# Kernel optimization log

Hardware: AMD Instinct MI355X
Metric: run time of the kernel (lower is better)

## Reference

```python
import jax, jax.numpy as jnp
import numpy as np

N_NODES = 100000
N_EDGES = 800000
IN_FEATS = 128
OUT_FEATS = 128
RANK_DIM = 128
NUM_BOND_TYPES = 32


def setup_inputs() -> dict:
    key = jax.random.key(0)
    ks = jax.random.split(key, 8)
    feat = jax.random.normal(ks[0], (N_NODES, IN_FEATS), dtype=jnp.float32)
    src = jax.random.randint(ks[1], (N_EDGES,), 0, N_NODES)
    dst = jax.random.randint(ks[2], (N_EDGES,), 0, N_NODES)
    # guarantee every node has in-degree >= 1 (module forbids 0-in-degree nodes)
    dst = dst.at[:N_NODES].set(jnp.arange(N_NODES))
    edge_attr = jax.random.randint(ks[3], (N_EDGES,), 0, NUM_BOND_TYPES)
    # xavier-uniform-like params
    def xavier(k, shape):
        lim = float(np.sqrt(6.0 / (shape[0] + shape[1])))
        return jax.random.uniform(k, shape, jnp.float32, -lim, lim)
    w1 = xavier(ks[4], (IN_FEATS, OUT_FEATS))
    w2 = xavier(ks[5], (IN_FEATS + 1, RANK_DIM))
    v = xavier(ks[6], (RANK_DIM, OUT_FEATS))
    bond_emb = jax.random.normal(ks[7], (NUM_BOND_TYPES, OUT_FEATS), dtype=jnp.float32)
    return {"feat": feat, "src": src, "dst": dst, "edge_attr": edge_attr,
            "w1": w1, "w2": w2, "v": v, "bond_emb": bond_emb}


def reference(feat, src, dst, edge_attr, w1, w2, v, bond_emb):
    N = feat.shape[0]
    E = src.shape[0]
    ones_e = jnp.ones((E,), dtype=feat.dtype)
    # norm == 'both': scale source features by out_degree^{-1/2}
    out_deg = jnp.clip(jax.ops.segment_sum(ones_e, src, num_segments=N), 1.0)
    feat_src = feat * (out_deg ** -0.5)[:, None]
    # two small GEMMs on node features
    h_sum = feat_src @ w1  # [N, out]
    feat_aug = jnp.concatenate([feat_src, jnp.ones((N, 1), dtype=feat.dtype)], axis=1)
    h_prod = jnp.tanh(feat_aug @ w2)  # [N, rank]
    # edge embedding (BondEncoder)
    ew = bond_emb[edge_attr]  # [E, out]
    # u_mul_e then neighbor-wise product / sum reductions onto dst
    m_prod = h_prod[src] * ew
    m_sum = h_sum[src] * ew
    hp = jax.ops.segment_prod(m_prod, dst, num_segments=N)
    hs = jax.ops.segment_sum(m_sum, dst, num_segments=N)
    rst = hs + hp @ v
    # norm == 'both': scale result by in_degree^{-1/2}
    in_deg = jnp.clip(jax.ops.segment_sum(ones_e, dst, num_segments=N), 1.0)
    rst = rst * (in_deg ** -0.5)[:, None]
    return rst
```

## Files before the change

kernel.cpp:

```cpp
#include <hip/hip_runtime.h>

#define N_NODES 100000
#define N_EDGES 800000

typedef unsigned short u16;
typedef unsigned int u32;
typedef __attribute__((ext_vector_type(8))) short short8;
typedef __attribute__((ext_vector_type(4))) float floatx4;

#define NBUK 196
#define BSH 9
#define NBLK 782
#define NB_PREPW 192

__device__ __forceinline__ float bflo(u32 u) {
    union { u32 i; float f; } v; v.i = u << 16; return v.f;
}
__device__ __forceinline__ float bfhi(u32 u) {
    union { u32 i; float f; } v; v.i = u & 0xFFFF0000u; return v.f;
}
__device__ __forceinline__ u16 f2bf(float f) {
    union { float f; u32 i; } v; v.f = f;
    u32 r = (v.i + 0x7FFFu + ((v.i >> 16) & 1u)) >> 16;
    return (u16)r;
}
__device__ __forceinline__ float fast_tanh(float x) {
    float e = __expf(2.0f * x);
    return 1.0f - 2.0f * __builtin_amdgcn_rcpf(e + 1.0f);
}


__global__ __launch_bounds__(256) void kA_count(const int* __restrict__ src, const int* __restrict__ dst,
                                                int* __restrict__ countsD, int* __restrict__ countsS,
                                                const float* __restrict__ w1, const float* __restrict__ w2,
                                                const float* __restrict__ v, u16* __restrict__ wvfrag) {
    __shared__ int cd[NBUK], cs[NBUK];
    if (blockIdx.x >= NBLK) {
        int idx = (blockIdx.x - NBLK) * 256 + threadIdx.x;
        if (idx < 3 * 16384) {
            int m = idx >> 14, r = idx & 16383;
            int k = r >> 7, o = r & 127;
            float val = (m == 0) ? w1[k * 128 + o] : (m == 1) ? w2[k * 128 + o] : v[k * 128 + o];
            int ot = o >> 4, ks = k >> 5, quad = (k >> 3) & 3, j = k & 7;
            int lane = (quad << 4) | (o & 15);
            wvfrag[(((m * 8 + ot) * 4 + ks) * 64 + lane) * 8 + j] = f2bf(val);
        }
        return;
    }
    for (int i = threadIdx.x; i < NBUK; i += 256) { cd[i] = 0; cs[i] = 0; }
    __syncthreads();
    int e4 = (blockIdx.x * 256 + threadIdx.x) * 4;
    if (e4 < N_EDGES) {
        int4 d4 = *(const int4*)(dst + e4);
        int4 s4 = *(const int4*)(src + e4);
        atomicAdd(&cd[d4.x >> BSH], 1); atomicAdd(&cd[d4.y >> BSH], 1);
        atomicAdd(&cd[d4.z >> BSH], 1); atomicAdd(&cd[d4.w >> BSH], 1);
        atomicAdd(&cs[s4.x >> BSH], 1); atomicAdd(&cs[s4.y >> BSH], 1);
        atomicAdd(&cs[s4.z >> BSH], 1); atomicAdd(&cs[s4.w >> BSH], 1);
    }
    __syncthreads();
    for (int i = threadIdx.x; i < NBUK; i += 256) {
        countsD[i * NBLK + blockIdx.x] = cd[i];
        countsS[i * NBLK + blockIdx.x] = cs[i];
    }
}


__global__ __launch_bounds__(256) void kA_scan(int* __restrict__ countsD, int* __restrict__ countsS,
                                               int* __restrict__ totD, int* __restrict__ totS) {
    __shared__ int sc[256];
    int b = blockIdx.x;
    int* cnt = (b < NBUK) ? (countsD + b * NBLK) : (countsS + (b - NBUK) * NBLK);
    int t = threadIdx.x;
    int v[4]; int s = 0;
#pragma unroll
    for (int j = 0; j < 4; j++) { int idx = t * 4 + j; v[j] = (idx < NBLK) ? cnt[idx] : 0; s += v[j]; }
    sc[t] = s; __syncthreads();
    for (int off = 1; off < 256; off <<= 1) {
        int x = (t >= off) ? sc[t - off] : 0;
        __syncthreads();
        sc[t] += x;
        __syncthreads();
    }
    int run = sc[t] - s;
#pragma unroll
    for (int j = 0; j < 4; j++) { int idx = t * 4 + j; if (idx < NBLK) { cnt[idx] = run; run += v[j]; } }
    if (t == 255) { if (b < NBUK) totD[b] = sc[255]; else totS[b - NBUK] = sc[255]; }
}


__global__ __launch_bounds__(256) void kA_scanT(const int* __restrict__ totD, const int* __restrict__ totS,
                                                int* __restrict__ baseD, int* __restrict__ baseS) {
    __shared__ int sd[256], ss[256];
    int t = threadIdx.x;
    int vd = (t < NBUK) ? totD[t] : 0;
    int vs = (t < NBUK) ? totS[t] : 0;
    sd[t] = vd; ss[t] = vs; __syncthreads();
    for (int off = 1; off < 256; off <<= 1) {
        int xd = (t >= off) ? sd[t - off] : 0;
        int xs = (t >= off) ? ss[t - off] : 0;
        __syncthreads();
        sd[t] += xd; ss[t] += xs;
        __syncthreads();
    }
    if (t < NBUK) { baseD[t] = sd[t] - vd; baseS[t] = ss[t] - vs; }
}


__global__ __launch_bounds__(256) void kA_scatter(const int* __restrict__ src, const int* __restrict__ dst,
                                                  const int* __restrict__ attr,
                                                  const int* __restrict__ countsD, const int* __restrict__ countsS,
                                                  const int* __restrict__ baseD, const int* __restrict__ baseS,
                                                  uint2* __restrict__ dbuf, int* __restrict__ sbuf) {
    __shared__ int curD[NBUK], curS[NBUK];
    for (int i = threadIdx.x; i < NBUK; i += 256) {
        curD[i] = baseD[i] + countsD[i * NBLK + blockIdx.x];
        curS[i] = baseS[i] + countsS[i * NBLK + blockIdx.x];
    }
    __syncthreads();
    int e4 = (blockIdx.x * 256 + threadIdx.x) * 4;
    if (e4 < N_EDGES) {
        int4 s4 = *(const int4*)(src + e4);
        int4 d4 = *(const int4*)(dst + e4);
        int4 a4 = *(const int4*)(attr + e4);
        int p, d, s, a;
        d = d4.x; s = s4.x; a = a4.x;
        p = atomicAdd(&curD[d >> BSH], 1); dbuf[p] = make_uint2((u32)d, (u32)((s << 5) | a));
        p = atomicAdd(&curS[s >> BSH], 1); sbuf[p] = s;
        d = d4.y; s = s4.y; a = a4.y;
        p = atomicAdd(&curD[d >> BSH], 1); dbuf[p] = make_uint2((u32)d, (u32)((s << 5) | a));
        p = atomicAdd(&curS[s >> BSH], 1); sbuf[p] = s;
        d = d4.z; s = s4.z; a = a4.z;
        p = atomicAdd(&curD[d >> BSH], 1); dbuf[p] = make_uint2((u32)d, (u32)((s << 5) | a));
        p = atomicAdd(&curS[s >> BSH], 1); sbuf[p] = s;
        d = d4.w; s = s4.w; a = a4.w;
        p = atomicAdd(&curD[d >> BSH], 1); dbuf[p] = make_uint2((u32)d, (u32)((s << 5) | a));
        p = atomicAdd(&curS[s >> BSH], 1); sbuf[p] = s;
    }
}


__global__ __launch_bounds__(256) void k_build(const uint2* __restrict__ dbuf, const int* __restrict__ sbuf,
                                               const int* __restrict__ baseD, const int* __restrict__ totD,
                                               const int* __restrict__ baseS, const int* __restrict__ totS,
                                               int* __restrict__ csr_start, int* __restrict__ in_deg,
                                               float* __restrict__ in_scale, float* __restrict__ out_scale,
                                               int* __restrict__ csr_edge) {
    __shared__ int cnt[512];
    __shared__ int aux[512];
    __shared__ int sc[256];
    int t = threadIdx.x;
    if (blockIdx.x >= NBUK) {
        int b = blockIdx.x - NBUK; int nb0 = b << BSH;
        for (int i = t; i < 512; i += 256) cnt[i] = 0;
        __syncthreads();
        int st = baseS[b], n = totS[b];
        for (int i = st + t; i < st + n; i += 256) atomicAdd(&cnt[sbuf[i] - nb0], 1);
        __syncthreads();
        for (int s = t; s < 512; s += 256) {
            int node = nb0 + s;
            if (node < N_NODES) { int c = cnt[s]; if (c < 1) c = 1; out_scale[node] = rsqrtf((float)c); }
        }
        return;
    }
    int b = blockIdx.x; int nb0 = b << BSH;
    for (int i = t; i < 512; i += 256) cnt[i] = 0;
    __syncthreads();
    int st = baseD[b], n = totD[b];
    for (int i = st + t; i < st + n; i += 256) { uint2 r = dbuf[i]; atomicAdd(&cnt[(int)r.x - nb0], 1); }
    __syncthreads();
    int c0 = cnt[2 * t], c1 = cnt[2 * t + 1];
    int s = c0 + c1; sc[t] = s; __syncthreads();
    for (int off = 1; off < 256; off <<= 1) {
        int x = (t >= off) ? sc[t - off] : 0;
        __syncthreads();
        sc[t] += x;
        __syncthreads();
    }
    int excl = sc[t] - s;
    aux[2 * t] = excl; aux[2 * t + 1] = excl + c0;
    int na = nb0 + 2 * t, nbv = nb0 + 2 * t + 1;
    if (na < N_NODES) {
        in_deg[na] = c0; int cc = c0 < 1 ? 1 : c0;
        in_scale[na] = rsqrtf((float)cc); csr_start[na] = st + excl;
    }
    if (nbv < N_NODES) {
        in_deg[nbv] = c1; int cc = c1 < 1 ? 1 : c1;
        in_scale[nbv] = rsqrtf((float)cc); csr_start[nbv] = st + excl + c0;
    }
    __syncthreads();
    for (int i = st + t; i < st + n; i += 256) {
        uint2 r = dbuf[i];
        int pos = atomicAdd(&aux[(int)r.x - nb0], 1);
        csr_edge[st + pos] = (int)r.y;
    }
}


__global__ __launch_bounds__(256) void k_gemm(const float* __restrict__ feat,
                                              const float* __restrict__ out_scale,
                                              const u16* __restrict__ wvfrag,
                                              const float* __restrict__ w2,
                                              u16* __restrict__ hrow) {
    __shared__ u16 ldsw[32768];
    for (int i = threadIdx.x; i < 4096; i += 256)
        ((ulonglong2*)ldsw)[i] = ((const ulonglong2*)wvfrag)[i];
    __syncthreads();
    int wave = threadIdx.x >> 6, lane = threadIdx.x & 63;
    int quad = lane >> 4, l15 = lane & 15;
    const float* bias = w2 + 128 * 128;
    float bias_v[8];
#pragma unroll
    for (int ot = 0; ot < 8; ot++) bias_v[ot] = bias[ot * 16 + l15];
    const int NT = (N_NODES + 63) / 64;
    for (int tile = blockIdx.x; tile < NT; tile += gridDim.x) {
        int nb = tile * 64 + wave * 16;
        int anode = nb + l15; if (anode >= N_NODES) anode = N_NODES - 1;
        float s = out_scale[anode];
        short8 a[4];
#pragma unroll
        for (int ks = 0; ks < 4; ks++) {
            float4 f0 = *(const float4*)(feat + anode * 128 + ks * 32 + quad * 8);
            float4 f1 = *(const float4*)(feat + anode * 128 + ks * 32 + quad * 8 + 4);
            short8 av;
            av[0] = (short)f2bf(f0.x * s); av[1] = (short)f2bf(f0.y * s);
            av[2] = (short)f2bf(f0.z * s); av[3] = (short)f2bf(f0.w * s);
            av[4] = (short)f2bf(f1.x * s); av[5] = (short)f2bf(f1.y * s);
            av[6] = (short)f2bf(f1.z * s); av[7] = (short)f2bf(f1.w * s);
            a[ks] = av;
        }
#pragma unroll
        for (int ot = 0; ot < 8; ot++) {
            floatx4 accS = (floatx4){0.f, 0.f, 0.f, 0.f};
            floatx4 accP = (floatx4){0.f, 0.f, 0.f, 0.f};
#pragma unroll
            for (int ks = 0; ks < 4; ks++) {
                short8 b0 = *(const short8*)&ldsw[((ot * 4 + ks) * 64 + lane) * 8];
                short8 b1 = *(const short8*)&ldsw[16384 + ((ot * 4 + ks) * 64 + lane) * 8];
                accS = __builtin_amdgcn_mfma_f32_16x16x32_bf16(a[ks], b0, accS, 0, 0, 0);
                accP = __builtin_amdgcn_mfma_f32_16x16x32_bf16(a[ks], b1, accP, 0, 0, 0);
            }
            int o = ot * 16 + l15;
#pragma unroll
            for (int r = 0; r < 4; r++) {
                int node = nb + quad * 4 + r;
                if (node < N_NODES) {
                    u32 pv = (u32)f2bf(accS[r]) | ((u32)f2bf(fast_tanh(accP[r] + bias_v[ot])) << 16);
                    *(u32*)(hrow + node * 256 + o * 2) = pv;
                }
            }
        }
    }
}


__global__ __launch_bounds__(256, 8) void k_edge(const int* __restrict__ csr_start, const int* __restrict__ in_deg,
                                                 const int* __restrict__ csr_edge,
                                                 const u16* __restrict__ hrow,
                                                 const float* __restrict__ bond_emb,
                                                 float* __restrict__ out_hs, u16* __restrict__ hp) {
    int wid = (blockIdx.x * 256 + threadIdx.x) >> 6;
    int lane = threadIdx.x & 63;
    int nwaves = (gridDim.x * 256) >> 6;
    const int NPAIR = N_NODES / 2;
    uint2 hC0 = {0, 0}, hC1 = {0, 0};
    float2 eC0 = {0.f, 0.f}, eC1 = {0.f, 0.f};
    for (int pr = wid; pr < NPAIR; pr += nwaves) {
        int n0 = pr * 2, n1 = n0 + 1;
        int st0 = csr_start[n0];
        int2 dd = *(const int2*)(in_deg + n0);
        int d0 = dd.x, d1 = dd.y;
        int st1 = st0 + d0;
        float as0 = 0.f, as1 = 0.f, ap0 = 1.f, ap1 = 1.f;
        float bs0 = 0.f, bs1 = 0.f, bp0 = 1.f, bp1 = 1.f;
        int b0 = 0, b1 = 0;
        while (b0 < d0 || b1 < d1) {
            int c0 = d0 - b0; c0 = c0 < 0 ? 0 : (c0 > 64 ? 64 : c0);
            int c1 = d1 - b1; c1 = c1 < 0 ? 0 : (c1 > 64 ? 64 : c1);
            int pkv0 = 0, pkv1 = 0;
            if (c0 > 0) { int li = lane < c0 ? lane : c0 - 1; pkv0 = csr_edge[st0 + b0 + li]; }
            if (c1 > 0) { int li = lane < c1 ? lane : c1 - 1; pkv1 = csr_edge[st1 + b1 + li]; }
            uint2 hA0 = hC0, hB0 = hC0, hA1 = hC1, hB1 = hC1;
            float2 eA0 = eC0, eB0 = eC0, eA1 = eC1, eB1 = eC1;
            if (c0 > 0) {
                int pk = __builtin_amdgcn_readlane(pkv0, 0);
                hA0 = *(const uint2*)(hrow + (pk >> 5) * 256 + 4 * lane);
                eA0 = *(const float2*)(bond_emb + (pk & 31) * 128 + 2 * lane);
                if (c0 > 1) {
                    pk = __builtin_amdgcn_readlane(pkv0, 1);
                    hB0 = *(const uint2*)(hrow + (pk >> 5) * 256 + 4 * lane);
                    eB0 = *(const float2*)(bond_emb + (pk & 31) * 128 + 2 * lane);
                }
            }
            if (c1 > 0) {
                int pk = __builtin_amdgcn_readlane(pkv1, 0);
                hA1 = *(const uint2*)(hrow + (pk >> 5) * 256 + 4 * lane);
                eA1 = *(const float2*)(bond_emb + (pk & 31) * 128 + 2 * lane);
                if (c1 > 1) {
                    pk = __builtin_amdgcn_readlane(pkv1, 1);
                    hB1 = *(const uint2*)(hrow + (pk >> 5) * 256 + 4 * lane);
                    eB1 = *(const float2*)(bond_emb + (pk & 31) * 128 + 2 * lane);
                }
            }
            int cm = c0 > c1 ? c0 : c1;
            for (int j = 0; j < cm; j++) {
                int jn = j + 2;
                if (jn < c0) {
                    int pk = __builtin_amdgcn_readlane(pkv0, jn);
                    hC0 = *(const uint2*)(hrow + (pk >> 5) * 256 + 4 * lane);
                    eC0 = *(const float2*)(bond_emb + (pk & 31) * 128 + 2 * lane);
                }
                if (jn < c1) {
                    int pk = __builtin_amdgcn_readlane(pkv1, jn);
                    hC1 = *(const uint2*)(hrow + (pk >> 5) * 256 + 4 * lane);
                    eC1 = *(const float2*)(bond_emb + (pk & 31) * 128 + 2 * lane);
                }
                if (j < c0) {
                    as0 += bflo(hA0.x) * eA0.x;
                    ap0 *= bfhi(hA0.x) * eA0.x;
                    as1 += bflo(hA0.y) * eA0.y;
                    ap1 *= bfhi(hA0.y) * eA0.y;
                    hA0 = hB0; eA0 = eB0; hB0 = hC0; eB0 = eC0;
                }
                if (j < c1) {
                    bs0 += bflo(hA1.x) * eA1.x;
                    bp0 *= bfhi(hA1.x) * eA1.x;
                    bs1 += bflo(hA1.y) * eA1.y;
                    bp1 *= bfhi(hA1.y) * eA1.y;
                    hA1 = hB1; eA1 = eB1; hB1 = hC1; eB1 = eC1;
                }
            }
            b0 += 64; b1 += 64;
        }
        float2 sv0; sv0.x = as0; sv0.y = as1;
        float2 sv1; sv1.x = bs0; sv1.y = bs1;
        *(float2*)(out_hs + n0 * 128 + 2 * lane) = sv0;
        *(float2*)(out_hs + n1 * 128 + 2 * lane) = sv1;
        *(u32*)(hp + n0 * 128 + 2 * lane) = ((u32)f2bf(ap1) << 16) | (u32)f2bf(ap0);
        *(u32*)(hp + n1 * 128 + 2 * lane) = ((u32)f2bf(bp1) << 16) | (u32)f2bf(bp0);
    }
}


__global__ __launch_bounds__(256) void k_final(const u16* __restrict__ hp,
                                               const u16* __restrict__ vfrag,
                                               const float* __restrict__ in_scale,
                                               float* __restrict__ out) {
    __shared__ u16 ldsw[16384];
    for (int i = threadIdx.x; i < 2048; i += 256)
        ((ulonglong2*)ldsw)[i] = ((const ulonglong2*)vfrag)[i];
    __syncthreads();
    int wave = threadIdx.x >> 6, lane = threadIdx.x & 63;
    int quad = lane >> 4, l15 = lane & 15;
    const int NT = (N_NODES + 63) / 64;
    for (int tile = blockIdx.x; tile < NT; tile += gridDim.x) {
        int nb = tile * 64 + wave * 16;
        int anode = nb + l15; if (anode >= N_NODES) anode = N_NODES - 1;
        short8 a[4];
#pragma unroll
        for (int ks = 0; ks < 4; ks++)
            a[ks] = *(const short8*)(hp + anode * 128 + ks * 32 + quad * 8);
#pragma unroll
        for (int ot = 0; ot < 8; ot++) {
            floatx4 acc = (floatx4){0.f, 0.f, 0.f, 0.f};
#pragma unroll
            for (int ks = 0; ks < 4; ks++) {
                short8 b = *(const short8*)&ldsw[((ot * 4 + ks) * 64 + lane) * 8];
                acc = __builtin_amdgcn_mfma_f32_16x16x32_bf16(a[ks], b, acc, 0, 0, 0);
            }
            int o = ot * 16 + l15;
#pragma unroll
            for (int r = 0; r < 4; r++) {
                int node = nb + quad * 4 + r;
                if (node < N_NODES) {
                    float scl = in_scale[node];
                    float hsv = out[node * 128 + o];
                    out[node * 128 + o] = (acc[r] + hsv) * scl;
                }
            }
        }
    }
}

extern "C" void kernel_launch(void* const* d_in, const int* in_sizes, int n_in,
                              void* d_out, int out_size, void* d_ws, size_t ws_size,
                              hipStream_t stream) {
    const float* feat = (const float*)d_in[0];
    const int* src = (const int*)d_in[1];
    const int* dst = (const int*)d_in[2];
    const int* attr = (const int*)d_in[3];
    const float* w1 = (const float*)d_in[4];
    const float* w2 = (const float*)d_in[5];
    const float* v = (const float*)d_in[6];
    const float* bond = (const float*)d_in[7];
    float* out = (float*)d_out;

    char* ws = (char*)d_ws;
    size_t off = 0;
    auto alloc = [&](size_t bytes) -> char* {
        char* p = ws + off; off += (bytes + 255) & ~(size_t)255; return p;
    };
    int* countsD   = (int*)alloc((size_t)NBUK * NBLK * 4);
    int* countsS   = (int*)alloc((size_t)NBUK * NBLK * 4);
    int* totD      = (int*)alloc((size_t)NBUK * 4);
    int* totS      = (int*)alloc((size_t)NBUK * 4);
    int* baseD     = (int*)alloc((size_t)NBUK * 4);
    int* baseS     = (int*)alloc((size_t)NBUK * 4);
    uint2* dbuf    = (uint2*)alloc((size_t)N_EDGES * 8);
    int* sbuf      = (int*)alloc((size_t)N_EDGES * 4);
    int* csr_start = (int*)alloc((size_t)N_NODES * 4);
    int* in_deg    = (int*)alloc((size_t)N_NODES * 4);
    float* out_scale = (float*)alloc((size_t)N_NODES * 4);
    float* in_scale  = (float*)alloc((size_t)N_NODES * 4);
    int* csr_edge  = (int*)alloc((size_t)N_EDGES * 4);
    u16* wvfrag = (u16*)alloc((size_t)3 * 16384 * 2);
    u16* hrow   = (u16*)alloc((size_t)N_NODES * 256 * 2);
    u16* hp     = (u16*)alloc((size_t)N_NODES * 128 * 2);

    (void)in_sizes; (void)n_in; (void)out_size; (void)ws_size;

    kA_count<<<NBLK + NB_PREPW, 256, 0, stream>>>(src, dst, countsD, countsS, w1, w2, v, wvfrag);
    kA_scan<<<2 * NBUK, 256, 0, stream>>>(countsD, countsS, totD, totS);
    kA_scanT<<<1, 256, 0, stream>>>(totD, totS, baseD, baseS);
    kA_scatter<<<NBLK, 256, 0, stream>>>(src, dst, attr, countsD, countsS, baseD, baseS, dbuf, sbuf);
    k_build<<<2 * NBUK, 256, 0, stream>>>(dbuf, sbuf, baseD, totD, baseS, totS,
                                          csr_start, in_deg, in_scale, out_scale, csr_edge);
    k_gemm<<<512, 256, 0, stream>>>(feat, out_scale, wvfrag, w2, hrow);
    k_edge<<<2048, 256, 0, stream>>>(csr_start, in_deg, csr_edge, hrow, bond, out, hp);
    k_final<<<1280, 256, 0, stream>>>(hp, wvfrag + 2 * 16384, in_scale, out);
}
```

Before: 302.6 us.

## Fold bucket-total scan into scatter/build kernels and cache bond embeddings in LDS

Removes the single-block kA_scanT launch. Each scatter block now recomputes the bucket-total prefix itself, and each build block computes its own base with a wave reduction. The count/scatter grid shrinks to 512 blocks, each looping over a 391-int4 edge chunk, so the per-bucket scan reads two entries per thread with no bounds checks. k_edge stages the 32x128 bond embedding table in shared memory instead of reading it from global memory for every edge. The cost is redundant scan work in every block and a 16KB LDS allocation per edge block, which may lower occupancy.

```diff
diff --git a/kernel.cpp b/kernel.cpp
--- a/kernel.cpp
+++ b/kernel.cpp
@@ -10,7 +10,9 @@
 
 #define NBUK 196
 #define BSH 9
-#define NBLK 782
+#define NBLK 512
+#define NE4 (N_EDGES / 4)
+#define CE 391
 #define NB_PREPW 192
 
 __device__ __forceinline__ float bflo(u32 u) {
@@ -49,10 +51,11 @@
     }
     for (int i = threadIdx.x; i < NBUK; i += 256) { cd[i] = 0; cs[i] = 0; }
     __syncthreads();
-    int e4 = (blockIdx.x * 256 + threadIdx.x) * 4;
-    if (e4 < N_EDGES) {
-        int4 d4 = *(const int4*)(dst + e4);
-        int4 s4 = *(const int4*)(src + e4);
+    int i0 = blockIdx.x * CE;
+    int i1 = i0 + CE; if (i1 > NE4) i1 = NE4;
+    for (int i = i0 + threadIdx.x; i < i1; i += 256) {
+        int4 d4 = ((const int4*)dst)[i];
+        int4 s4 = ((const int4*)src)[i];
         atomicAdd(&cd[d4.x >> BSH], 1); atomicAdd(&cd[d4.y >> BSH], 1);
         atomicAdd(&cd[d4.z >> BSH], 1); atomicAdd(&cd[d4.w >> BSH], 1);
         atomicAdd(&cs[s4.x >> BSH], 1); atomicAdd(&cs[s4.y >> BSH], 1);
@@ -72,9 +75,8 @@
     int b = blockIdx.x;
     int* cnt = (b < NBUK) ? (countsD + b * NBLK) : (countsS + (b - NBUK) * NBLK);
     int t = threadIdx.x;
-    int v[4]; int s = 0;
-#pragma unroll
-    for (int j = 0; j < 4; j++) { int idx = t * 4 + j; v[j] = (idx < NBLK) ? cnt[idx] : 0; s += v[j]; }
+    int v0 = cnt[2 * t], v1 = cnt[2 * t + 1];
+    int s = v0 + v1;
     sc[t] = s; __syncthreads();
     for (int off = 1; off < 256; off <<= 1) {
         int x = (t >= off) ? sc[t - off] : 0;
@@ -82,15 +84,18 @@
         sc[t] += x;
         __syncthreads();
     }
-    int run = sc[t] - s;
-#pragma unroll
-    for (int j = 0; j < 4; j++) { int idx = t * 4 + j; if (idx < NBLK) { cnt[idx] = run; run += v[j]; } }
+    int excl = sc[t] - s;
+    cnt[2 * t] = excl; cnt[2 * t + 1] = excl + v0;
     if (t == 255) { if (b < NBUK) totD[b] = sc[255]; else totS[b - NBUK] = sc[255]; }
 }
 
 
-__global__ __launch_bounds__(256) void kA_scanT(const int* __restrict__ totD, const int* __restrict__ totS,
-                                                int* __restrict__ baseD, int* __restrict__ baseS) {
+__global__ __launch_bounds__(256) void kA_scatter(const int* __restrict__ src, const int* __restrict__ dst,
+                                                  const int* __restrict__ attr,
+                                                  const int* __restrict__ countsD, const int* __restrict__ countsS,
+                                                  const int* __restrict__ totD, const int* __restrict__ totS,
+                                                  uint2* __restrict__ dbuf, int* __restrict__ sbuf) {
+    __shared__ int curD[NBUK], curS[NBUK];
     __shared__ int sd[256], ss[256];
     int t = threadIdx.x;
     int vd = (t < NBUK) ? totD[t] : 0;
@@ -103,26 +108,17 @@
         sd[t] += xd; ss[t] += xs;
         __syncthreads();
     }
-    if (t < NBUK) { baseD[t] = sd[t] - vd; baseS[t] = ss[t] - vs; }
-}
-
-
-__global__ __launch_bounds__(256) void kA_scatter(const int* __restrict__ src, const int* __restrict__ dst,
-                                                  const int* __restrict__ attr,
-                                                  const int* __restrict__ countsD, const int* __restrict__ countsS,
-                                                  const int* __restrict__ baseD, const int* __restrict__ baseS,
-                                                  uint2* __restrict__ dbuf, int* __restrict__ sbuf) {
-    __shared__ int curD[NBUK], curS[NBUK];
-    for (int i = threadIdx.x; i < NBUK; i += 256) {
-        curD[i] = baseD[i] + countsD[i * NBLK + blockIdx.x];
-        curS[i] = baseS[i] + countsS[i * NBLK + blockIdx.x];
-    }
-    __syncthreads();
-    int e4 = (blockIdx.x * 256 + threadIdx.x) * 4;
-    if (e4 < N_EDGES) {
-        int4 s4 = *(const int4*)(src + e4);
-        int4 d4 = *(const int4*)(dst + e4);
-        int4 a4 = *(const int4*)(attr + e4);
+    if (t < NBUK) {
+        curD[t] = (sd[t] - vd) + countsD[t * NBLK + blockIdx.x];
+        curS[t] = (ss[t] - vs) + countsS[t * NBLK + blockIdx.x];
+    }
+    __syncthreads();
+    int i0 = blockIdx.x * CE;
+    int i1 = i0 + CE; if (i1 > NE4) i1 = NE4;
+    for (int i = i0 + t; i < i1; i += 256) {
+        int4 s4 = ((const int4*)src)[i];
+        int4 d4 = ((const int4*)dst)[i];
+        int4 a4 = ((const int4*)attr)[i];
         int p, d, s, a;
         d = d4.x; s = s4.x; a = a4.x;
         p = atomicAdd(&curD[d >> BSH], 1); dbuf[p] = make_uint2((u32)d, (u32)((s << 5) | a));
@@ -141,32 +137,38 @@
 
 
 __global__ __launch_bounds__(256) void k_build(const uint2* __restrict__ dbuf, const int* __restrict__ sbuf,
-                                               const int* __restrict__ baseD, const int* __restrict__ totD,
-                                               const int* __restrict__ baseS, const int* __restrict__ totS,
+                                               const int* __restrict__ totD, const int* __restrict__ totS,
                                                int* __restrict__ csr_start, int* __restrict__ in_deg,
                                                float* __restrict__ in_scale, float* __restrict__ out_scale,
                                                int* __restrict__ csr_edge) {
     __shared__ int cnt[512];
     __shared__ int aux[512];
     __shared__ int sc[256];
+    __shared__ int sbase;
     int t = threadIdx.x;
-    if (blockIdx.x >= NBUK) {
-        int b = blockIdx.x - NBUK; int nb0 = b << BSH;
-        for (int i = t; i < 512; i += 256) cnt[i] = 0;
-        __syncthreads();
-        int st = baseS[b], n = totS[b];
+    int isS = blockIdx.x >= NBUK;
+    int b = isS ? (blockIdx.x - NBUK) : blockIdx.x;
+    const int* tot = isS ? totS : totD;
+    if (t < 64) {
+        int s = 0;
+        for (int i = t; i < b; i += 64) s += tot[i];
+#pragma unroll
+        for (int o = 32; o > 0; o >>= 1) s += __shfl_down(s, o);
+        if (t == 0) sbase = s;
+    }
+    for (int i = t; i < 512; i += 256) cnt[i] = 0;
+    __syncthreads();
+    int st = sbase, n = tot[b];
+    int nb0 = b << BSH;
+    if (isS) {
         for (int i = st + t; i < st + n; i += 256) atomicAdd(&cnt[sbuf[i] - nb0], 1);
         __syncthreads();
-        for (int s = t; s < 512; s += 256) {
-            int node = nb0 + s;
-            if (node < N_NODES) { int c = cnt[s]; if (c < 1) c = 1; out_scale[node] = rsqrtf((float)c); }
+        for (int s2 = t; s2 < 512; s2 += 256) {
+            int node = nb0 + s2;
+            if (node < N_NODES) { int c = cnt[s2]; if (c < 1) c = 1; out_scale[node] = rsqrtf((float)c); }
         }
         return;
     }
-    int b = blockIdx.x; int nb0 = b << BSH;
-    for (int i = t; i < 512; i += 256) cnt[i] = 0;
-    __syncthreads();
-    int st = baseD[b], n = totD[b];
     for (int i = st + t; i < st + n; i += 256) { uint2 r = dbuf[i]; atomicAdd(&cnt[(int)r.x - nb0], 1); }
     __syncthreads();
     int c0 = cnt[2 * t], c1 = cnt[2 * t + 1];
@@ -259,6 +261,9 @@
                                                  const u16* __restrict__ hrow,
                                                  const float* __restrict__ bond_emb,
                                                  float* __restrict__ out_hs, u16* __restrict__ hp) {
+    __shared__ float ldsb[4096];
+    for (int i = threadIdx.x; i < 4096; i += 256) ldsb[i] = bond_emb[i];
+    __syncthreads();
     int wid = (blockIdx.x * 256 + threadIdx.x) >> 6;
     int lane = threadIdx.x & 63;
     int nwaves = (gridDim.x * 256) >> 6;
@@ -285,21 +290,21 @@
             if (c0 > 0) {
                 int pk = __builtin_amdgcn_readlane(pkv0, 0);
                 hA0 = *(const uint2*)(hrow + (pk >> 5) * 256 + 4 * lane);
-                eA0 = *(const float2*)(bond_emb + (pk & 31) * 128 + 2 * lane);
+                eA0 = *(const float2*)&ldsb[(pk & 31) * 128 + 2 * lane];
                 if (c0 > 1) {
                     pk = __builtin_amdgcn_readlane(pkv0, 1);
                     hB0 = *(const uint2*)(hrow + (pk >> 5) * 256 + 4 * lane);
-                    eB0 = *(const float2*)(bond_emb + (pk & 31) * 128 + 2 * lane);
+                    eB0 = *(const float2*)&ldsb[(pk & 31) * 128 + 2 * lane];
                 }
             }
             if (c1 > 0) {
                 int pk = __builtin_amdgcn_readlane(pkv1, 0);
                 hA1 = *(const uint2*)(hrow + (pk >> 5) * 256 + 4 * lane);
-                eA1 = *(const float2*)(bond_emb + (pk & 31) * 128 + 2 * lane);
+                eA1 = *(const float2*)&ldsb[(pk & 31) * 128 + 2 * lane];
                 if (c1 > 1) {
                     pk = __builtin_amdgcn_readlane(pkv1, 1);
                     hB1 = *(const uint2*)(hrow + (pk >> 5) * 256 + 4 * lane);
-                    eB1 = *(const float2*)(bond_emb + (pk & 31) * 128 + 2 * lane);
+                    eB1 = *(const float2*)&ldsb[(pk & 31) * 128 + 2 * lane];
                 }
             }
             int cm = c0 > c1 ? c0 : c1;
@@ -308,12 +313,12 @@
                 if (jn < c0) {
                     int pk = __builtin_amdgcn_readlane(pkv0, jn);
                     hC0 = *(const uint2*)(hrow + (pk >> 5) * 256 + 4 * lane);
-                    eC0 = *(const float2*)(bond_emb + (pk & 31) * 128 + 2 * lane);
+                    eC0 = *(const float2*)&ldsb[(pk & 31) * 128 + 2 * lane];
                 }
                 if (jn < c1) {
                     int pk = __builtin_amdgcn_readlane(pkv1, jn);
                     hC1 = *(const uint2*)(hrow + (pk >> 5) * 256 + 4 * lane);
-                    eC1 = *(const float2*)(bond_emb + (pk & 31) * 128 + 2 * lane);
+                    eC1 = *(const float2*)&ldsb[(pk & 31) * 128 + 2 * lane];
                 }
                 if (j < c0) {
                     as0 += bflo(hA0.x) * eA0.x;
@@ -404,8 +409,6 @@
     int* countsS   = (int*)alloc((size_t)NBUK * NBLK * 4);
     int* totD      = (int*)alloc((size_t)NBUK * 4);
     int* totS      = (int*)alloc((size_t)NBUK * 4);
-    int* baseD     = (int*)alloc((size_t)NBUK * 4);
-    int* baseS     = (int*)alloc((size_t)NBUK * 4);
     uint2* dbuf    = (uint2*)alloc((size_t)N_EDGES * 8);
     int* sbuf      = (int*)alloc((size_t)N_EDGES * 4);
     int* csr_start = (int*)alloc((size_t)N_NODES * 4);
@@ -421,9 +424,8 @@
 
     kA_count<<<NBLK + NB_PREPW, 256, 0, stream>>>(src, dst, countsD, countsS, w1, w2, v, wvfrag);
     kA_scan<<<2 * NBUK, 256, 0, stream>>>(countsD, countsS, totD, totS);
-    kA_scanT<<<1, 256, 0, stream>>>(totD, totS, baseD, baseS);
-    kA_scatter<<<NBLK, 256, 0, stream>>>(src, dst, attr, countsD, countsS, baseD, baseS, dbuf, sbuf);
-    k_build<<<2 * NBUK, 256, 0, stream>>>(dbuf, sbuf, baseD, totD, baseS, totS,
+    kA_scatter<<<NBLK, 256, 0, stream>>>(src, dst, attr, countsD, countsS, totD, totS, dbuf, sbuf);
+    k_build<<<2 * NBUK, 256, 0, stream>>>(dbuf, sbuf, totD, totS,
                                           csr_start, in_deg, in_scale, out_scale, csr_edge);
     k_gemm<<<512, 256, 0, stream>>>(feat, out_scale, wvfrag, w2, hrow);
     k_edge<<<2048, 256, 0, stream>>>(csr_start, in_deg, csr_edge, hrow, bond, out, hp);
```

Measured after the change: 295.4 us. -2.4%, faster.
